# Kernel tuning notes

Measured on AMD Instinct MI355X. Metric: run time of the kernel, lower is better.

The kernel has to match this reference:

```python
import jax, jax.numpy as jnp
import numpy as np

KERNEL_SIZE = 3  # from init_kwargs


def median_blur(x, k=KERNEL_SIZE):
    # cv2.medianBlur uses replicated (edge) borders; output same shape as input.
    pad = k // 2
    B, H, W, C = x.shape
    xp = jnp.pad(x, ((0, 0), (pad, pad), (pad, pad), (0, 0)), mode='edge')
    # Gather the k*k shifted views -> [B, H, W, C, k*k]
    patches = jnp.stack(
        [xp[:, i:i + H, j:j + W, :] for i in range(k) for j in range(k)],
        axis=-1,
    )
    return jnp.median(patches, axis=-1)


def setup_inputs() -> dict:
    key = jax.random.key(0)
    # image-like values in [0, 255); median is an order statistic so scale is faithful
    input_batch = jax.random.uniform(key, (32, 512, 512, 3), dtype=jnp.float32) * 255.0
    return {"input_batch": input_batch}


def reference(input_batch):
    # Faithful JAX version of Blurring(blurring_type='median', kernel_size=3):
    # per-pixel median over the 3x3 neighborhood with replicate border,
    # computed batched instead of per-image cv2 on host.
    # (uint8 cast omitted to keep a float path; same order-statistic math.)
    return median_blur(input_batch)
```

## Files before the change

kernel.cpp:

```cpp
#include <hip/hip_runtime.h>


#define IMG_H 512
#define IMG_W 512
#define IMG_C 3
#define ROW_F (IMG_W * IMG_C)
#define NGROUPS (ROW_F / 4)
#define TILE_H 8

__device__ __forceinline__ float med3f(float a, float b, float c) {
    return __builtin_amdgcn_fmed3f(a, b, c);
}
__device__ __forceinline__ float min3f(float a, float b, float c) {
    return fminf(fminf(a, b), c);
}
__device__ __forceinline__ float max3f(float a, float b, float c) {
    return fmaxf(fmaxf(a, b), c);
}

__device__ __forceinline__ float4 min3v(float4 a, float4 b, float4 c) {
    return make_float4(min3f(a.x,b.x,c.x), min3f(a.y,b.y,c.y),
                       min3f(a.z,b.z,c.z), min3f(a.w,b.w,c.w));
}
__device__ __forceinline__ float4 med3v(float4 a, float4 b, float4 c) {
    return make_float4(med3f(a.x,b.x,c.x), med3f(a.y,b.y,c.y),
                       med3f(a.z,b.z,c.z), med3f(a.w,b.w,c.w));
}
__device__ __forceinline__ float4 max3v(float4 a, float4 b, float4 c) {
    return make_float4(max3f(a.x,b.x,c.x), max3f(a.y,b.y,c.y),
                       max3f(a.z,b.z,c.z), max3f(a.w,b.w,c.w));
}

__global__ __launch_bounds__(128) void median3x3_kernel(
        const float* __restrict__ in, float* __restrict__ out) {
    const int g  = blockIdx.x * blockDim.x + threadIdx.x;
    const int b  = blockIdx.z;
    const int h0 = blockIdx.y * TILE_H;

    const bool left_edge  = (g == 0);
    const bool right_edge = (g == NGROUPS - 1);

    const float* base  = in  + (size_t)b * IMG_H * ROW_F + (size_t)g * 4;
    float*       obase = out + (size_t)b * IMG_H * ROW_F + (size_t)g * 4;

    float4 mn0, md0, mx0, mn1, md1, mx1, mn2, md2, mx2;

    auto loadrow = [&](int r, float4& mn, float4& md, float4& mx) {
        const float* p = base + (size_t)r * ROW_F;
        const float4 mb = *(const float4*)p;
        float4 l, rr;
        if (!left_edge) {
            const float4 lb = *(const float4*)(p - 4);
            l = make_float4(lb.y, lb.z, lb.w, mb.x);
        } else {
            l = make_float4(mb.x, mb.y, mb.z, mb.x);
        }
        if (!right_edge) {
            const float4 rb = *(const float4*)(p + 4);
            rr = make_float4(mb.w, rb.x, rb.y, rb.z);
        } else {
            rr = make_float4(mb.w, mb.y, mb.z, mb.w);
        }
        mn = min3v(l, mb, rr);
        md = med3v(l, mb, rr);
        mx = max3v(l, mb, rr);
    };

    loadrow((h0 == 0) ? 0 : h0 - 1, mn0, md0, mx0);
    loadrow(h0, mn1, md1, mx1);

    #pragma unroll
    for (int i = 0; i < TILE_H; ++i) {
        const int h  = h0 + i;
        const int hp = (h == IMG_H - 1) ? h : h + 1;
        loadrow(hp, mn2, md2, mx2);

        const float4 A  = max3v(mn0, mn1, mn2);
        const float4 Bm = med3v(md0, md1, md2);
        const float4 Cm = min3v(mx0, mx1, mx2);
        *(float4*)(obase + (size_t)h * ROW_F) = med3v(A, Bm, Cm);

        mn0 = mn1; md0 = md1; mx0 = mx1;
        mn1 = mn2; md1 = md2; mx1 = mx2;
    }
}

extern "C" void kernel_launch(void* const* d_in, const int* in_sizes, int n_in,
                              void* d_out, int out_size, void* d_ws, size_t ws_size,
                              hipStream_t stream) {
    const float* in = (const float*)d_in[0];
    float* out = (float*)d_out;

    const int B = in_sizes[0] / (IMG_H * ROW_F);

    dim3 grid(NGROUPS / 128, IMG_H / TILE_H, B);
    dim3 block(128, 1, 1);
    median3x3_kernel<<<grid, block, 0, stream>>>(in, out);
}
```

Baseline: 187.7 us.

## Compute one output row per thread and use nontemporal stores

Drops the per-thread vertical sliding window over eight rows, so each thread now loads its three input rows and writes a single output row, with a grid that has one block per image row. The goal is more memory-level parallelism, since all nine loads are issued up front, and outputs are written with nontemporal stores so they do not pollute the cache. In exchange, each input row is now loaded by three different threads and the row min/median/max work is repeated, so more cache traffic and more blocks are launched.

```diff
diff --git a/kernel.cpp b/kernel.cpp
--- a/kernel.cpp
+++ b/kernel.cpp
@@ -6,7 +6,8 @@
 #define IMG_C 3
 #define ROW_F (IMG_W * IMG_C)
 #define NGROUPS (ROW_F / 4)
-#define TILE_H 8
+
+typedef float floatx4 __attribute__((ext_vector_type(4)));
 
 __device__ __forceinline__ float med3f(float a, float b, float c) {
     return __builtin_amdgcn_fmed3f(a, b, c);
@@ -33,56 +34,62 @@
 
 __global__ __launch_bounds__(128) void median3x3_kernel(
         const float* __restrict__ in, float* __restrict__ out) {
-    const int g  = blockIdx.x * blockDim.x + threadIdx.x;
-    const int b  = blockIdx.z;
-    const int h0 = blockIdx.y * TILE_H;
+    const int g = blockIdx.x * blockDim.x + threadIdx.x;
+    const int h = blockIdx.y;
+    const int b = blockIdx.z;
 
     const bool left_edge  = (g == 0);
     const bool right_edge = (g == NGROUPS - 1);
 
-    const float* base  = in  + (size_t)b * IMG_H * ROW_F + (size_t)g * 4;
-    float*       obase = out + (size_t)b * IMG_H * ROW_F + (size_t)g * 4;
+    const int hm = (h == 0)         ? 0 : h - 1;
+    const int hp = (h == IMG_H - 1) ? h : h + 1;
 
-    float4 mn0, md0, mx0, mn1, md1, mx1, mn2, md2, mx2;
+    const float* base = in + (size_t)b * IMG_H * ROW_F + (size_t)g * 4;
+    const float* p0 = base + (size_t)hm * ROW_F;
+    const float* p1 = base + (size_t)h  * ROW_F;
+    const float* p2 = base + (size_t)hp * ROW_F;
 
-    auto loadrow = [&](int r, float4& mn, float4& md, float4& mx) {
-        const float* p = base + (size_t)r * ROW_F;
-        const float4 mb = *(const float4*)p;
-        float4 l, rr;
-        if (!left_edge) {
-            const float4 lb = *(const float4*)(p - 4);
-            l = make_float4(lb.y, lb.z, lb.w, mb.x);
-        } else {
-            l = make_float4(mb.x, mb.y, mb.z, mb.x);
-        }
-        if (!right_edge) {
-            const float4 rb = *(const float4*)(p + 4);
-            rr = make_float4(mb.w, rb.x, rb.y, rb.z);
-        } else {
-            rr = make_float4(mb.w, mb.y, mb.z, mb.w);
-        }
-        mn = min3v(l, mb, rr);
-        md = med3v(l, mb, rr);
-        mx = max3v(l, mb, rr);
-    };
+    const float4 m0 = *(const float4*)p0;
+    const float4 m1 = *(const float4*)p1;
+    const float4 m2 = *(const float4*)p2;
+    float4 l0, l1, l2, r0, r1, r2;
+    if (!left_edge) {
+        const float4 a0 = *(const float4*)(p0 - 4);
+        const float4 a1 = *(const float4*)(p1 - 4);
+        const float4 a2 = *(const float4*)(p2 - 4);
+        l0 = make_float4(a0.y, a0.z, a0.w, m0.x);
+        l1 = make_float4(a1.y, a1.z, a1.w, m1.x);
+        l2 = make_float4(a2.y, a2.z, a2.w, m2.x);
+    } else {
+        l0 = make_float4(m0.x, m0.y, m0.z, m0.x);
+        l1 = make_float4(m1.x, m1.y, m1.z, m1.x);
+        l2 = make_float4(m2.x, m2.y, m2.z, m2.x);
+    }
+    if (!right_edge) {
+        const float4 c0 = *(const float4*)(p0 + 4);
+        const float4 c1 = *(const float4*)(p1 + 4);
+        const float4 c2 = *(const float4*)(p2 + 4);
+        r0 = make_float4(m0.w, c0.x, c0.y, c0.z);
+        r1 = make_float4(m1.w, c1.x, c1.y, c1.z);
+        r2 = make_float4(m2.w, c2.x, c2.y, c2.z);
+    } else {
+        r0 = make_float4(m0.w, m0.y, m0.z, m0.w);
+        r1 = make_float4(m1.w, m1.y, m1.z, m1.w);
+        r2 = make_float4(m2.w, m2.y, m2.z, m2.w);
+    }
 
-    loadrow((h0 == 0) ? 0 : h0 - 1, mn0, md0, mx0);
-    loadrow(h0, mn1, md1, mx1);
+    const float4 mn0 = min3v(l0, m0, r0), md0 = med3v(l0, m0, r0), mx0 = max3v(l0, m0, r0);
+    const float4 mn1 = min3v(l1, m1, r1), md1 = med3v(l1, m1, r1), mx1 = max3v(l1, m1, r1);
+    const float4 mn2 = min3v(l2, m2, r2), md2 = med3v(l2, m2, r2), mx2 = max3v(l2, m2, r2);
 
-    #pragma unroll
-    for (int i = 0; i < TILE_H; ++i) {
-        const int h  = h0 + i;
-        const int hp = (h == IMG_H - 1) ? h : h + 1;
-        loadrow(hp, mn2, md2, mx2);
+    const float4 A  = max3v(mn0, mn1, mn2);
+    const float4 Bm = med3v(md0, md1, md2);
+    const float4 Cm = min3v(mx0, mx1, mx2);
+    const float4 res = med3v(A, Bm, Cm);
 
-        const float4 A  = max3v(mn0, mn1, mn2);
-        const float4 Bm = med3v(md0, md1, md2);
-        const float4 Cm = min3v(mx0, mx1, mx2);
-        *(float4*)(obase + (size_t)h * ROW_F) = med3v(A, Bm, Cm);
-
-        mn0 = mn1; md0 = md1; mx0 = mx1;
-        mn1 = mn2; md1 = md2; mx1 = mx2;
-    }
+    float* op = out + (size_t)b * IMG_H * ROW_F + (size_t)h * ROW_F + (size_t)g * 4;
+    floatx4 rv = { res.x, res.y, res.z, res.w };
+    __builtin_nontemporal_store(rv, (floatx4*)op);
 }
 
 extern "C" void kernel_launch(void* const* d_in, const int* in_sizes, int n_in,
@@ -93,7 +100,7 @@
 
     const int B = in_sizes[0] / (IMG_H * ROW_F);
 
-    dim3 grid(NGROUPS / 128, IMG_H / TILE_H, B);
+    dim3 grid(NGROUPS / 128, IMG_H, B);
     dim3 block(128, 1, 1);
     median3x3_kernel<<<grid, block, 0, stream>>>(in, out);
 }
```

Result: slower. 206.7 us (+10.1%).

## Stage halo tiles in LDS with XCD-aware block remap and nontemporal stores

Applied to the files above, without the earlier changes.

Each 256-thread block now loads a 10x66 float4 halo tile (clamped borders) into shared memory, then each thread computes two output rows from LDS using the separable min/med/max 3x3 median network. The 1D grid is remapped so that consecutive block IDs spread images across the 8 XCDs, keeping each image's halo reuse within one XCD's L2. Outputs use nontemporal stores to avoid polluting cache. This adds a sync and LDS traffic, plus extra halo reads (10 rows per 8 output rows), in place of the old per-thread streaming over rows held in registers.

```diff
diff --git a/kernel.cpp b/kernel.cpp
--- a/kernel.cpp
+++ b/kernel.cpp
@@ -6,7 +6,14 @@
 #define IMG_C 3
 #define ROW_F (IMG_W * IMG_C)
 #define NGROUPS (ROW_F / 4)
-#define TILE_H 8
+
+#define TW 64
+#define TH 8
+#define SROWS (TH + 2)
+#define SGROUPS (TW + 2)
+#define STRIDE 268
+
+typedef float floatx4 __attribute__((ext_vector_type(4)));
 
 __device__ __forceinline__ float med3f(float a, float b, float c) {
     return __builtin_amdgcn_fmed3f(a, b, c);
@@ -31,57 +38,74 @@
                        max3f(a.z,b.z,c.z), max3f(a.w,b.w,c.w));
 }
 
-__global__ __launch_bounds__(128) void median3x3_kernel(
+__global__ __launch_bounds__(256) void median3x3_kernel(
         const float* __restrict__ in, float* __restrict__ out) {
-    const int g  = blockIdx.x * blockDim.x + threadIdx.x;
-    const int b  = blockIdx.z;
-    const int h0 = blockIdx.y * TILE_H;
+    __shared__ float lds[SROWS * STRIDE];
 
-    const bool left_edge  = (g == 0);
-    const bool right_edge = (g == NGROUPS - 1);
+    const int l   = blockIdx.x;
+    const int xcd = l & 7;
+    const int s   = l >> 3;
+    const int hy  = s & 63;
+    const int t2  = s >> 6;
+    const int bx  = t2 % 6;
+    const int img = t2 / 6;
+    const int b   = xcd + 8 * img;
 
-    const float* base  = in  + (size_t)b * IMG_H * ROW_F + (size_t)g * 4;
-    float*       obase = out + (size_t)b * IMG_H * ROW_F + (size_t)g * 4;
+    const int h0 = hy * TH;
+    const int G0 = bx * TW;
 
-    float4 mn0, md0, mx0, mn1, md1, mx1, mn2, md2, mx2;
+    const float* ibase = in + (size_t)b * IMG_H * ROW_F;
+    for (int k = threadIdx.x; k < SROWS * SGROUPS; k += 256) {
+        const int rr = k / SGROUPS;
+        const int kk = k - rr * SGROUPS;
+        int h = h0 - 1 + rr;
+        h = (h < 0) ? 0 : ((h > IMG_H - 1) ? IMG_H - 1 : h);
+        int gg = G0 - 1 + kk;
+        gg = (gg < 0) ? 0 : ((gg > NGROUPS - 1) ? NGROUPS - 1 : gg);
+        const float4 v = *(const float4*)(ibase + (size_t)h * ROW_F + (size_t)gg * 4);
+        *(float4*)(&lds[rr * STRIDE + kk * 4]) = v;
+    }
+    __syncthreads();
 
-    auto loadrow = [&](int r, float4& mn, float4& md, float4& mx) {
-        const float* p = base + (size_t)r * ROW_F;
-        const float4 mb = *(const float4*)p;
-        float4 l, rr;
+    const int tx = threadIdx.x & 63;
+    const int ty = threadIdx.x >> 6;
+    const int r0 = ty * 2;
+
+    const bool left_edge  = (bx == 0 && tx == 0);
+    const bool right_edge = (bx == 5 && tx == TW - 1);
+
+    float4 mn[4], md[4], mx[4];
+    #pragma unroll
+    for (int i = 0; i < 4; ++i) {
+        const float* row = &lds[(r0 + i) * STRIDE + (tx + 1) * 4];
+        const float4 m = *(const float4*)row;
+        float4 lv, rv;
         if (!left_edge) {
-            const float4 lb = *(const float4*)(p - 4);
-            l = make_float4(lb.y, lb.z, lb.w, mb.x);
+            const float4 lb = *(const float4*)(row - 4);
+            lv = make_float4(lb.y, lb.z, lb.w, m.x);
         } else {
-            l = make_float4(mb.x, mb.y, mb.z, mb.x);
+            lv = make_float4(m.x, m.y, m.z, m.x);
         }
         if (!right_edge) {
-            const float4 rb = *(const float4*)(p + 4);
-            rr = make_float4(mb.w, rb.x, rb.y, rb.z);
+            const float4 rb = *(const float4*)(row + 4);
+            rv = make_float4(m.w, rb.x, rb.y, rb.z);
         } else {
-            rr = make_float4(mb.w, mb.y, mb.z, mb.w);
+            rv = make_float4(m.w, m.y, m.z, m.w);
         }
-        mn = min3v(l, mb, rr);
-        md = med3v(l, mb, rr);
-        mx = max3v(l, mb, rr);
-    };
+        mn[i] = min3v(lv, m, rv);
+        md[i] = med3v(lv, m, rv);
+        mx[i] = max3v(lv, m, rv);
+    }
 
-    loadrow((h0 == 0) ? 0 : h0 - 1, mn0, md0, mx0);
-    loadrow(h0, mn1, md1, mx1);
-
+    float* obase = out + (size_t)b * IMG_H * ROW_F + (size_t)G0 * 4 + (size_t)tx * 4;
     #pragma unroll
-    for (int i = 0; i < TILE_H; ++i) {
-        const int h  = h0 + i;
-        const int hp = (h == IMG_H - 1) ? h : h + 1;
-        loadrow(hp, mn2, md2, mx2);
-
-        const float4 A  = max3v(mn0, mn1, mn2);
-        const float4 Bm = med3v(md0, md1, md2);
-        const float4 Cm = min3v(mx0, mx1, mx2);
-        *(float4*)(obase + (size_t)h * ROW_F) = med3v(A, Bm, Cm);
-
-        mn0 = mn1; md0 = md1; mx0 = mx1;
-        mn1 = mn2; md1 = md2; mx1 = mx2;
+    for (int j = 0; j < 2; ++j) {
+        const float4 A  = max3v(mn[j], mn[j+1], mn[j+2]);
+        const float4 Bm = med3v(md[j], md[j+1], md[j+2]);
+        const float4 Cm = min3v(mx[j], mx[j+1], mx[j+2]);
+        const float4 res = med3v(A, Bm, Cm);
+        floatx4 rv4 = { res.x, res.y, res.z, res.w };
+        __builtin_nontemporal_store(rv4, (floatx4*)(obase + (size_t)(h0 + r0 + j) * ROW_F));
     }
 }
 
@@ -92,8 +116,7 @@
     float* out = (float*)d_out;
 
     const int B = in_sizes[0] / (IMG_H * ROW_F);
+    const int nblocks = B * (IMG_H / TH) * (NGROUPS / TW);
 
-    dim3 grid(NGROUPS / 128, IMG_H / TILE_H, B);
-    dim3 block(128, 1, 1);
-    median3x3_kernel<<<grid, block, 0, stream>>>(in, out);
+    median3x3_kernel<<<dim3(nblocks, 1, 1), dim3(256, 1, 1), 0, stream>>>(in, out);
 }
```

Measured after the change: 176.7 us. -5.9%, faster.
